# Optimization experiments

Hardware: AMD Instinct MI355X
Metric: run time of the kernel (lower is better)

Reference implementation:

```python
import jax, jax.numpy as jnp
import numpy as np
from jax import lax

N_PTS = 256          # hardcoded point count in original loops
BIG = 257.0 ** 2     # initial SE sentinel in original code


def setup_inputs() -> dict:
    key = jax.random.key(0)
    k1, k2 = jax.random.split(key)
    B = 2048
    inp = jax.random.normal(k1, (B, 1, 2 * N_PTS), dtype=jnp.float32)
    tgt = jax.random.normal(k2, (B, 1, 2 * N_PTS), dtype=jnp.float32)
    return {"input": inp, "targets": tgt}


def reference(input, targets):
    B = input.shape[0]
    # interleaved (x, y) pairs -> [B, 256, 2]
    pin = input[:, 0, :].reshape(B, N_PTS, 2)
    ptg = targets[:, 0, :].reshape(B, N_PTS, 2)
    # pairwise squared distances: D[b, j, k] = ||tgt_j - in_k||^2
    D = jnp.sum((ptg[:, :, None, :] - pin[:, None, :, :]) ** 2, axis=-1)  # [B,256,256]
    big = jnp.asarray(BIG, dtype=D.dtype)
    batch_idx = jnp.arange(B)

    def step(used, dj):
        # dj: [B, 256] distances from target point j to all input points
        vals = jnp.where(used, jnp.inf, dj)
        m = jnp.min(vals, axis=1)
        k = jnp.argmin(vals, axis=1)
        se = jnp.minimum(m, big)              # SE stays 257^2 if nothing beats it
        k = jnp.where(m < big, k, 0)          # k_tmp stays 0 in that case
        used = used.at[batch_idx, k].set(True)
        return used, se

    used0 = jnp.zeros((B, N_PTS), dtype=bool)
    _, ses = lax.scan(step, used0, jnp.swapaxes(D, 0, 1))  # iterate j=0..255, ses: [256, B]
    loss = jnp.sum(ses) / B / (2 * N_PTS)
    return loss
```

## Files before the change

kernel.cpp:

```cpp
#include <hip/hip_runtime.h>
#include <stdint.h>

#define N_PTS 256

typedef unsigned long long ull;
typedef float v2f __attribute__((ext_vector_type(2)));

__device__ __forceinline__ unsigned umin2(unsigned a, unsigned b) { return a < b ? a : b; }

template<int CTRL>
__device__ __forceinline__ unsigned dppmax(unsigned x) {
    unsigned y = (unsigned)__builtin_amdgcn_update_dpp(0, (int)x, CTRL, 0xf, 0xf, true);
    return x > y ? x : y;
}

__device__ __forceinline__ unsigned wave_cmax(float m) {
    unsigned c = ~__float_as_uint(m);
    c = dppmax<0x121>(c);
    c = dppmax<0x122>(c);
    c = dppmax<0x124>(c);
    c = dppmax<0x128>(c);
    c = dppmax<0x142>(c);
    c = dppmax<0x143>(c);
    return ~((unsigned)__builtin_amdgcn_readlane((int)c, 63));
}

__device__ __forceinline__ void round1(
    float tjx, float tjy, unsigned lane, float& acc,
    v2f& p0, v2f& p1, v2f& p2, v2f& p3, float vNAN)
{
    #pragma clang fp contract(off)
    v2f t; t.x = tjx; t.y = tjy;
    v2f q0 = t - p0, q1 = t - p1, q2 = t - p2, q3 = t - p3;
    v2f s0 = q0 * q0, s1 = q1 * q1, s2 = q2 * q2, s3 = q3 * q3;
    float d0 = s0.x + s0.y;
    float d1 = s1.x + s1.y;
    float d2 = s2.x + s2.y;
    float d3 = s3.x + s3.y;

    float m = fminf(fminf(d0, d1), fminf(d2, d3));
    unsigned mu = wave_cmax(m);
    float ms = __uint_as_float(mu);

    ull e0 = __ballot(d0 == ms);
    ull e1 = __ballot(d1 == ms);
    ull e2 = __ballot(d2 == ms);
    ull e3 = __ballot(d3 == ms);
    unsigned u0 = (unsigned)(__ffsll((long long)e0) - 1);
    unsigned u1 = ((unsigned)(__ffsll((long long)e1) - 1)) | 64u;
    unsigned u2 = ((unsigned)(__ffsll((long long)e2) - 1)) | 128u;
    unsigned u3 = ((unsigned)(__ffsll((long long)e3) - 1)) | 192u;
    unsigned k  = umin2(umin2(u0, u1), umin2(u2, u3));

    const unsigned BIG_U = __float_as_uint(66049.0f);
    bool ok = (mu < BIG_U);
    k = ok ? k : 0u;
    unsigned se = umin2(mu, BIG_U);
    acc += __uint_as_float(se);

    unsigned ks = k >> 6, kl = k & 63u;
    bool hit = (lane == kl);
    p0.x = (hit && ks == 0) ? vNAN : p0.x;
    p1.x = (hit && ks == 1) ? vNAN : p1.x;
    p2.x = (hit && ks == 2) ? vNAN : p2.x;
    p3.x = (hit && ks == 3) ? vNAN : p3.x;
}

__device__ __forceinline__ void phase(
    float txc, float tyc, unsigned lane, float& acc,
    v2f& p0, v2f& p1, v2f& p2, v2f& p3, float vNAN)
{
    #pragma unroll 1
    for (int j = 0; j < 64; ++j) {
        float tjx = __int_as_float(__builtin_amdgcn_readlane(__float_as_int(txc), j));
        float tjy = __int_as_float(__builtin_amdgcn_readlane(__float_as_int(tyc), j));
        round1(tjx, tjy, lane, acc, p0, p1, p2, p3, vNAN);
    }
}

__global__ __launch_bounds__(256) void greedy_match_kernel(
    const float* __restrict__ input,
    const float* __restrict__ targets,
    float* __restrict__ out,
    int B, float scale)
{
    __shared__ float wsum[4];
    const unsigned lane = threadIdx.x & 63;
    const int wid  = threadIdx.x >> 6;
    const int b    = blockIdx.x * 4 + wid;

    float acc = 0.0f;
    if (b < B) {
        const v2f* pin = (const v2f*)(input   + (size_t)b * (2 * N_PTS));
        const v2f* ptg = (const v2f*)(targets + (size_t)b * (2 * N_PTS));

        v2f p0 = pin[lane],       p1 = pin[64 + lane];
        v2f p2 = pin[128 + lane], p3 = pin[192 + lane];
        v2f t0 = ptg[lane],       t1 = ptg[64 + lane];
        v2f t2 = ptg[128 + lane], t3 = ptg[192 + lane];

        const float vNAN = __int_as_float(0x7fc00000);

        phase(t0.x, t0.y, lane, acc, p0, p1, p2, p3, vNAN);
        phase(t1.x, t1.y, lane, acc, p0, p1, p2, p3, vNAN);
        phase(t2.x, t2.y, lane, acc, p0, p1, p2, p3, vNAN);
        phase(t3.x, t3.y, lane, acc, p0, p1, p2, p3, vNAN);
    }

    if (lane == 0) wsum[wid] = acc;
    __syncthreads();
    if (threadIdx.x == 0) {
        float s = (wsum[0] + wsum[1] + wsum[2] + wsum[3]) * scale;
        atomicAdd(out, s);
    }
}

extern "C" void kernel_launch(void* const* d_in, const int* in_sizes, int n_in,
                              void* d_out, int out_size, void* d_ws, size_t ws_size,
                              hipStream_t stream) {
    const float* input   = (const float*)d_in[0];
    const float* targets = (const float*)d_in[1];
    float* out = (float*)d_out;

    const int B = in_sizes[0] / (2 * N_PTS);
    const float scale = 1.0f / ((float)B * (float)(2 * N_PTS));

    hipMemsetAsync(d_out, 0, sizeof(float) * (size_t)out_size, stream);

    const int blocks = (B + 3) / 4;
    greedy_match_kernel<<<blocks, 256, 0, stream>>>(input, targets, out, B, scale);
}
```

Baseline: 120.8 us.

## Speculatively process two target points per iteration with conflict fallback

```diff
diff --git a/kernel.cpp b/kernel.cpp
--- a/kernel.cpp
+++ b/kernel.cpp
@@ -14,34 +14,29 @@
     return x > y ? x : y;
 }
 
-__device__ __forceinline__ unsigned wave_cmax(float m) {
+__device__ __forceinline__ unsigned wave_cmax1(float m) {
     unsigned c = ~__float_as_uint(m);
-    c = dppmax<0x121>(c);
-    c = dppmax<0x122>(c);
-    c = dppmax<0x124>(c);
-    c = dppmax<0x128>(c);
-    c = dppmax<0x142>(c);
-    c = dppmax<0x143>(c);
+    c = dppmax<0x121>(c); c = dppmax<0x122>(c); c = dppmax<0x124>(c);
+    c = dppmax<0x128>(c); c = dppmax<0x142>(c); c = dppmax<0x143>(c);
     return ~((unsigned)__builtin_amdgcn_readlane((int)c, 63));
 }
 
-__device__ __forceinline__ void round1(
-    float tjx, float tjy, unsigned lane, float& acc,
-    v2f& p0, v2f& p1, v2f& p2, v2f& p3, float vNAN)
-{
-    #pragma clang fp contract(off)
-    v2f t; t.x = tjx; t.y = tjy;
-    v2f q0 = t - p0, q1 = t - p1, q2 = t - p2, q3 = t - p3;
-    v2f s0 = q0 * q0, s1 = q1 * q1, s2 = q2 * q2, s3 = q3 * q3;
-    float d0 = s0.x + s0.y;
-    float d1 = s1.x + s1.y;
-    float d2 = s2.x + s2.y;
-    float d3 = s3.x + s3.y;
+__device__ __forceinline__ void wave_cmax2(float mA, float mB,
+                                           unsigned& muA, unsigned& muB) {
+    unsigned a = ~__float_as_uint(mA);
+    unsigned b = ~__float_as_uint(mB);
+    a = dppmax<0x121>(a); b = dppmax<0x121>(b);
+    a = dppmax<0x122>(a); b = dppmax<0x122>(b);
+    a = dppmax<0x124>(a); b = dppmax<0x124>(b);
+    a = dppmax<0x128>(a); b = dppmax<0x128>(b);
+    a = dppmax<0x142>(a); b = dppmax<0x142>(b);
+    a = dppmax<0x143>(a); b = dppmax<0x143>(b);
+    muA = ~((unsigned)__builtin_amdgcn_readlane((int)a, 63));
+    muB = ~((unsigned)__builtin_amdgcn_readlane((int)b, 63));
+}
 
-    float m = fminf(fminf(d0, d1), fminf(d2, d3));
-    unsigned mu = wave_cmax(m);
-    float ms = __uint_as_float(mu);
-
+__device__ __forceinline__ unsigned argmin_ballots(
+    float d0, float d1, float d2, float d3, float ms) {
     ull e0 = __ballot(d0 == ms);
     ull e1 = __ballot(d1 == ms);
     ull e2 = __ballot(d2 == ms);
@@ -50,14 +45,11 @@
     unsigned u1 = ((unsigned)(__ffsll((long long)e1) - 1)) | 64u;
     unsigned u2 = ((unsigned)(__ffsll((long long)e2) - 1)) | 128u;
     unsigned u3 = ((unsigned)(__ffsll((long long)e3) - 1)) | 192u;
-    unsigned k  = umin2(umin2(u0, u1), umin2(u2, u3));
+    return umin2(umin2(u0, u1), umin2(u2, u3));
+}
 
-    const unsigned BIG_U = __float_as_uint(66049.0f);
-    bool ok = (mu < BIG_U);
-    k = ok ? k : 0u;
-    unsigned se = umin2(mu, BIG_U);
-    acc += __uint_as_float(se);
-
+__device__ __forceinline__ void poison(unsigned k, unsigned lane, float vNAN,
+                                       v2f& p0, v2f& p1, v2f& p2, v2f& p3) {
     unsigned ks = k >> 6, kl = k & 63u;
     bool hit = (lane == kl);
     p0.x = (hit && ks == 0) ? vNAN : p0.x;
@@ -66,15 +58,59 @@
     p3.x = (hit && ks == 3) ? vNAN : p3.x;
 }
 
+#define DIST4(tx, ty, D0, D1, D2, D3)                                  \
+    {                                                                  \
+        v2f t; t.x = (tx); t.y = (ty);                                 \
+        v2f q0 = t - p0, q1 = t - p1, q2 = t - p2, q3 = t - p3;        \
+        v2f s0 = q0 * q0, s1 = q1 * q1, s2 = q2 * q2, s3 = q3 * q3;    \
+        D0 = s0.x + s0.y; D1 = s1.x + s1.y;                            \
+        D2 = s2.x + s2.y; D3 = s3.x + s3.y;                            \
+    }
+
 __device__ __forceinline__ void phase(
     float txc, float tyc, unsigned lane, float& acc,
     v2f& p0, v2f& p1, v2f& p2, v2f& p3, float vNAN)
 {
+    #pragma clang fp contract(off)
+    const unsigned BIG_U = __float_as_uint(66049.0f);
     #pragma unroll 1
-    for (int j = 0; j < 64; ++j) {
-        float tjx = __int_as_float(__builtin_amdgcn_readlane(__float_as_int(txc), j));
-        float tjy = __int_as_float(__builtin_amdgcn_readlane(__float_as_int(tyc), j));
-        round1(tjx, tjy, lane, acc, p0, p1, p2, p3, vNAN);
+    for (int j = 0; j < 64; j += 2) {
+        float tAx = __int_as_float(__builtin_amdgcn_readlane(__float_as_int(txc), j));
+        float tAy = __int_as_float(__builtin_amdgcn_readlane(__float_as_int(tyc), j));
+        float tBx = __int_as_float(__builtin_amdgcn_readlane(__float_as_int(txc), j + 1));
+        float tBy = __int_as_float(__builtin_amdgcn_readlane(__float_as_int(tyc), j + 1));
+
+        float dA0, dA1, dA2, dA3, dB0, dB1, dB2, dB3;
+        DIST4(tAx, tAy, dA0, dA1, dA2, dA3);
+        DIST4(tBx, tBy, dB0, dB1, dB2, dB3);
+
+        float mA = fminf(fminf(dA0, dA1), fminf(dA2, dA3));
+        float mB = fminf(fminf(dB0, dB1), fminf(dB2, dB3));
+        unsigned muA, muB;
+        wave_cmax2(mA, mB, muA, muB);
+        float msA = __uint_as_float(muA);
+        float msB = __uint_as_float(muB);
+
+        unsigned kA = argmin_ballots(dA0, dA1, dA2, dA3, msA);
+        unsigned kB = argmin_ballots(dB0, dB1, dB2, dB3, msB);
+
+        bool okA = (muA < BIG_U);
+        kA = okA ? kA : 0u;
+        acc += __uint_as_float(umin2(muA, BIG_U));
+        poison(kA, lane, vNAN, p0, p1, p2, p3);
+
+        if (kB == kA) {
+            float r0, r1, r2, r3;
+            DIST4(tBx, tBy, r0, r1, r2, r3);
+            float m2 = fminf(fminf(r0, r1), fminf(r2, r3));
+            muB = wave_cmax1(m2);
+            msB = __uint_as_float(muB);
+            kB = argmin_ballots(r0, r1, r2, r3, msB);
+        }
+        bool okB = (muB < BIG_U);
+        kB = okB ? kB : 0u;
+        acc += __uint_as_float(umin2(muB, BIG_U));
+        poison(kB, lane, vNAN, p0, p1, p2, p3);
     }
 }
 
```

Result: no change. 121.7 us (+0.8%).
